# Optimization experiments

Hardware: AMD Instinct MI355X
Metric: run time of the kernel (lower is better)

## Reference

```python
import jax, jax.numpy as jnp
import numpy as np


def setup_inputs() -> dict:
    key = jax.random.key(0)
    k1, k2, k3 = jax.random.split(key, 3)
    N, M, D = 8192, 8192, 64
    return {
        "query": jax.random.normal(k1, (N, D), dtype=jnp.float32),
        "key": jax.random.normal(k2, (M, D), dtype=jnp.float32),
        "value": jax.random.normal(k3, (M, D), dtype=jnp.float32),
        "hyper_c": 1,
        "num_of_method": 2,
    }


def reference(query, key, value, hyper_c, num_of_method):
    # num_of_method == 2 (default): cosine-similarity scores scaled by hyper_c.
    # L2-normalize rows (dim=1), matmul, scale, softmax over keys, weight values.
    q_norm = query / jnp.linalg.norm(query, axis=1, keepdims=True)
    k_norm = key / jnp.linalg.norm(key, axis=1, keepdims=True)
    scores = hyper_c * jnp.einsum("nd,md->nm", q_norm, k_norm)  # [N, M]
    p_attn = jax.nn.softmax(scores, axis=-1)
    res_query = jnp.einsum("nm,md->nd", p_attn, value)  # [N, D]
    return (res_query, p_attn)
```

## Files before the change

### kernel.cpp

```cpp
#include <hip/hip_runtime.h>
#include <hip/hip_bf16.h>
#include <cstdint>
#include <cstddef>

#define NQ 8192
#define NK 8192
#define DD 64
#define KSPLIT 4
#define KRANGE (NK / KSPLIT)
#define KTILE 128

typedef __bf16 bf16x8 __attribute__((ext_vector_type(8)));
typedef float f32x16 __attribute__((ext_vector_type(16)));
typedef unsigned short u16;
typedef uint32_t u32;

static __device__ __forceinline__ u16 f2bf(float f) {
    union { float f; uint32_t u; } v; v.f = f;
    uint32_t r = (v.u + 0x7fffu + ((v.u >> 16) & 1u)) >> 16;
    return (u16)r;
}

static __device__ __forceinline__ u32 cvtpk(float lo, float hi) {
    u32 r;
    asm("v_cvt_pk_bf16_f32 %0, %1, %2" : "=v"(r) : "v"(lo), "v"(hi));
    return r;
}

#define GLOAD16(g, l)                                                          \
    __builtin_amdgcn_global_load_lds(                                          \
        (__attribute__((address_space(1))) void*)(g),                          \
        (__attribute__((address_space(3))) void*)(l), 16, 0, 0)

__global__ void k_norm(const float* __restrict__ q, const float* __restrict__ k,
                       u16* __restrict__ qn, u16* __restrict__ kn) {
    int wid  = (blockIdx.x * blockDim.x + threadIdx.x) >> 6;
    int lane = threadIdx.x & 63;
    int nw   = (gridDim.x * blockDim.x) >> 6;
    for (int row = wid; row < 2 * NQ; row += nw) {
        const float* src = (row < NQ) ? q : k;
        u16* dst = (row < NQ) ? qn : kn;
        int r = row & (NQ - 1);
        float x = src[(size_t)r * DD + lane];
        float ss = x * x;
        #pragma unroll
        for (int m = 1; m < 64; m <<= 1) ss += __shfl_xor(ss, m, 64);
        dst[(size_t)r * DD + lane] = f2bf(x * rsqrtf(ss));
    }
}

__global__ void k_transv(const float* __restrict__ v, u16* __restrict__ vT) {
    __shared__ float ts[64][65];
    int mb = blockIdx.x * 64;
    int t = threadIdx.x;
    #pragma unroll
    for (int i = 0; i < 16; i++) {
        int idx = i * 256 + t;
        int r = idx >> 6, c = idx & 63;
        ts[r][c] = v[(size_t)(mb + r) * DD + c];
    }
    __syncthreads();
    #pragma unroll
    for (int i = 0; i < 16; i++) {
        int idx = i * 256 + t;
        int d = idx >> 6, m = idx & 63;
        vT[(size_t)d * NK + mb + m] = f2bf(ts[m][d]);
    }
}

__global__ __launch_bounds__(256) void
k_flash(const u16* __restrict__ qn, const u16* __restrict__ kn,
        const u16* __restrict__ vT, const int* __restrict__ hcp,
        float* __restrict__ prs, float* __restrict__ ppv) {
    __shared__ __align__(16) u16 qs[32 * 64];
    __shared__ __align__(16) union SmT {
        struct { u16 ks[128 * 64]; u16 vs[64 * 128]; } a;
        struct { float redA[32 * 64]; float redB[32 * 64]; } b;
    } sm;
    __shared__ float rs_ws[4][32];

    const float hc = (float)hcp[0];
    const int t = threadIdx.x;
    const int w = t >> 6;
    const int lane = t & 63;
    const int l31 = lane & 31;
    const int half = lane >> 5;
    const int qb = (blockIdx.x >> 2) * 32;
    const int sp = blockIdx.x & 3;
    const int k0 = sp * KRANGE;
    const int kw = w * 32;

    {
        int row = t >> 3, c = t & 7;
        *reinterpret_cast<uint4*>(&qs[row * 64 + ((c ^ (row & 7)) * 8)]) =
            *reinterpret_cast<const uint4*>(&qn[(size_t)(qb + row) * DD + c * 8]);
    }

    float rs_sum = 0.f;
    f32x16 pv0, pv1;
    #pragma unroll
    for (int i = 0; i < 16; i++) { pv0[i] = 0.f; pv1[i] = 0.f; }

    for (int kb = 0; kb < KRANGE / KTILE; kb++) {
        __syncthreads();
        const u16* ksrc = kn + (size_t)(k0 + kb * KTILE) * DD;
        #pragma unroll
        for (int i = 0; i < 4; i++) {
            int idx16 = (w * 4 + i) * 64 + lane;
            int row = idx16 >> 3, c = idx16 & 7;
            GLOAD16(ksrc + (size_t)row * DD + ((c ^ (row & 7)) * 8),
                    &sm.a.ks[(w * 4 + i) * 512]);
        }
        const u16* vsrc = vT + (size_t)(k0 + kb * KTILE);
        #pragma unroll
        for (int i = 0; i < 4; i++) {
            int idx16 = (w * 4 + i) * 64 + lane;
            int row = idx16 >> 4, c = idx16 & 15;
            GLOAD16(vsrc + (size_t)row * NK + ((c ^ (row & 7)) * 8),
                    &sm.a.vs[(w * 4 + i) * 512]);
        }
        __syncthreads();

        f32x16 acc;
        #pragma unroll
        for (int i = 0; i < 16; i++) acc[i] = 0.f;
        #pragma unroll
        for (int s = 0; s < 4; s++) {
            int ca = 2 * s + half;
            int kr = kw + l31;
            bf16x8 af = *reinterpret_cast<const bf16x8*>(&sm.a.ks[kr * 64 + ((ca ^ (kr & 7)) * 8)]);
            bf16x8 bf = *reinterpret_cast<const bf16x8*>(&qs[l31 * 64 + ((ca ^ (l31 & 7)) * 8)]);
            acc = __builtin_amdgcn_mfma_f32_32x32x16_bf16(af, bf, acc, 0, 0, 0);
        }
        float e[16];
        #pragma unroll
        for (int r = 0; r < 16; r++) {
            e[r] = __expf(acc[r] * hc);
            rs_sum += e[r];
        }
        bf16x8 pa[2];
        #pragma unroll
        for (int s = 0; s < 2; s++) {
            u32 x0 = cvtpk(e[8 * s + 0], e[8 * s + 1]);
            u32 y0 = cvtpk(e[8 * s + 4], e[8 * s + 5]);
            auto r0 = __builtin_amdgcn_permlane32_swap(x0, y0, false, false);
            u32 x1 = cvtpk(e[8 * s + 2], e[8 * s + 3]);
            u32 y1 = cvtpk(e[8 * s + 6], e[8 * s + 7]);
            auto r1 = __builtin_amdgcn_permlane32_swap(x1, y1, false, false);
            union { u32 u[4]; bf16x8 v; } f;
            f.u[0] = r0[0]; f.u[1] = r1[0]; f.u[2] = r0[1]; f.u[3] = r1[1];
            pa[s] = f.v;
        }
        #pragma unroll
        for (int s = 0; s < 2; s++) {
            int cv = (kw >> 3) + 2 * s + half;
            int vr0 = l31, vr1 = 32 + l31;
            bf16x8 b0 = *reinterpret_cast<const bf16x8*>(&sm.a.vs[vr0 * 128 + ((cv ^ (vr0 & 7)) * 8)]);
            bf16x8 b1 = *reinterpret_cast<const bf16x8*>(&sm.a.vs[vr1 * 128 + ((cv ^ (vr1 & 7)) * 8)]);
            pv0 = __builtin_amdgcn_mfma_f32_32x32x16_bf16(pa[s], b0, pv0, 0, 0, 0);
            pv1 = __builtin_amdgcn_mfma_f32_32x32x16_bf16(pa[s], b1, pv1, 0, 0, 0);
        }
    }

    rs_sum += __shfl_xor(rs_sum, 32, 64);
    if (lane < 32) rs_ws[w][lane] = rs_sum;
    __syncthreads();
    if (t < 32)
        prs[(size_t)sp * NQ + qb + t] =
            rs_ws[0][t] + rs_ws[1][t] + rs_ws[2][t] + rs_ws[3][t];

    float* redA = sm.b.redA;
    float* redB = sm.b.redB;
    if (w == 0) {
        #pragma unroll
        for (int r = 0; r < 16; r++) {
            int qq = (r & 3) + 8 * (r >> 2) + 4 * half;
            redA[qq * 64 + l31] = pv0[r];
            redA[qq * 64 + 32 + l31] = pv1[r];
        }
    } else if (w == 1) {
        #pragma unroll
        for (int r = 0; r < 16; r++) {
            int qq = (r & 3) + 8 * (r >> 2) + 4 * half;
            redB[qq * 64 + l31] = pv0[r];
            redB[qq * 64 + 32 + l31] = pv1[r];
        }
    }
    __syncthreads();
    if (w == 2) {
        #pragma unroll
        for (int r = 0; r < 16; r++) {
            int qq = (r & 3) + 8 * (r >> 2) + 4 * half;
            redA[qq * 64 + l31] += pv0[r];
            redA[qq * 64 + 32 + l31] += pv1[r];
        }
    } else if (w == 3) {
        #pragma unroll
        for (int r = 0; r < 16; r++) {
            int qq = (r & 3) + 8 * (r >> 2) + 4 * half;
            redB[qq * 64 + l31] += pv0[r];
            redB[qq * 64 + 32 + l31] += pv1[r];
        }
    }
    __syncthreads();
    float* dst = ppv + (size_t)sp * NQ * DD + (size_t)qb * DD;
    #pragma unroll
    for (int i = 0; i < 8; i++) {
        int idx = i * 256 + t;
        dst[idx] = redA[idx] + redB[idx];
    }
}

__global__ void k_reduce(const float* __restrict__ prs, const float* __restrict__ ppv,
                         float* __restrict__ inv_rs, float* __restrict__ out_res) {
    int id = blockIdx.x * blockDim.x + threadIdx.x;
    int n = id >> 6, d = id & 63;
    float s = prs[n] + prs[NQ + n] + prs[2 * NQ + n] + prs[3 * NQ + n];
    float inv = 1.0f / s;
    if (d == 0) inv_rs[n] = inv;
    const size_t st = (size_t)NQ * DD;
    float v = ppv[id] + ppv[st + id] + ppv[2 * st + id] + ppv[3 * st + id];
    out_res[id] = v * inv;
}

__global__ __launch_bounds__(256) void
k_pwrite(const u16* __restrict__ qn, const u16* __restrict__ kn,
         const float* __restrict__ inv_rs, const int* __restrict__ hcp,
         float* __restrict__ out_p) {
    __shared__ __align__(16) u16 qs2[64 * 64];
    __shared__ __align__(16) u16 ks2[64 * 64];
    __shared__ __align__(16) float pl[64 * 68];
    __shared__ float invl[64];

    const float hc = (float)hcp[0];
    const int bid = blockIdx.x;
    const int qb = (bid >> 7) * 64;
    const int kb = (bid & 127) * 64;
    const int t = threadIdx.x;
    const int w = t >> 6;
    const int lane = t & 63;
    const int l31 = lane & 31;
    const int half = lane >> 5;

    #pragma unroll
    for (int i = 0; i < 2; i++) {
        int idx16 = (w * 2 + i) * 64 + lane;
        int row = idx16 >> 3, c = idx16 & 7;
        GLOAD16(qn + (size_t)(qb + row) * DD + ((c ^ (row & 7)) * 8),
                &qs2[(w * 2 + i) * 512]);
        GLOAD16(kn + (size_t)(kb + row) * DD + ((c ^ (row & 7)) * 8),
                &ks2[(w * 2 + i) * 512]);
    }
    if (t < 64) invl[t] = inv_rs[qb + t];
    __syncthreads();

    const int wq = (w >> 1) * 32, wk = (w & 1) * 32;
    f32x16 acc;
    #pragma unroll
    for (int i = 0; i < 16; i++) acc[i] = 0.f;
    #pragma unroll
    for (int s = 0; s < 4; s++) {
        int ca = 2 * s + half;
        int qr = wq + l31, kr = wk + l31;
        bf16x8 a = *reinterpret_cast<const bf16x8*>(&qs2[qr * 64 + ((ca ^ (qr & 7)) * 8)]);
        bf16x8 b = *reinterpret_cast<const bf16x8*>(&ks2[kr * 64 + ((ca ^ (kr & 7)) * 8)]);
        acc = __builtin_amdgcn_mfma_f32_32x32x16_bf16(a, b, acc, 0, 0, 0);
    }
    #pragma unroll
    for (int r = 0; r < 16; r++) {
        int qq = wq + (r & 3) + 8 * (r >> 2) + 4 * half;
        pl[qq * 68 + wk + l31] = __expf(acc[r] * hc) * invl[qq];
    }
    __syncthreads();
    #pragma unroll
    for (int i = 0; i < 4; i++) {
        int idx = i * 256 + t;
        int row = idx >> 4, c4 = idx & 15;
        float4 vv = *reinterpret_cast<const float4*>(&pl[row * 68 + c4 * 4]);
        *reinterpret_cast<float4*>(&out_p[(size_t)(qb + row) * NK + kb + c4 * 4]) = vv;
    }
}

extern "C" void kernel_launch(void* const* d_in, const int* in_sizes, int n_in,
                              void* d_out, int out_size, void* d_ws, size_t ws_size,
                              hipStream_t stream) {
    const float* q = (const float*)d_in[0];
    const float* k = (const float*)d_in[1];
    const float* v = (const float*)d_in[2];
    const int* hc = (const int*)d_in[3];

    float* out_res = (float*)d_out;
    float* out_p = out_res + (size_t)NQ * DD;

    char* wsb = (char*)d_ws;
    u16* qn = (u16*)wsb;
    u16* kn = qn + (size_t)NQ * DD;
    u16* vT = kn + (size_t)NK * DD;
    float* inv_rs = (float*)(vT + (size_t)NK * DD);

    const size_t base_need = 3 * (size_t)NQ * DD * 2 + (size_t)NQ * 4;
    const size_t extra_need = (size_t)KSPLIT * NQ * 4 + (size_t)KSPLIT * NQ * DD * 4;
    char* extra = (ws_size >= base_need + extra_need)
                      ? wsb + base_need
                      : (char*)out_p + ((size_t)NQ * NK * 4 - extra_need);
    float* prs = (float*)extra;
    float* ppv = prs + (size_t)KSPLIT * NQ;

    k_norm<<<1024, 256, 0, stream>>>(q, k, qn, kn);
    k_transv<<<NK / 64, 256, 0, stream>>>(v, vT);
    k_flash<<<(NQ / 32) * KSPLIT, 256, 0, stream>>>(qn, kn, vT, hc, prs, ppv);
    k_reduce<<<(NQ * DD) / 256, 256, 0, stream>>>(prs, ppv, inv_rs, out_res);
    k_pwrite<<<(NQ / 64) * (NK / 64), 256, 0, stream>>>(qn, kn, inv_rs, hc, out_p);
}
```

Before: 333.8 us.

## Double-buffer K/V tiles in flash kernel and store P directly from registers

The flash kernel now keeps two K/V shared-memory buffers and issues the next tile's loads before computing on the current one, so global loads overlap the MFMA work, with one barrier per iteration instead of two. Doubling the buffers raises LDS use, and launch bounds now ask for 2 blocks per CU. The P-write kernel drops its LDS staging tile and writes exp values straight from MFMA accumulators to global memory with scalar 4-byte stores, and asks for 4 blocks per CU. The direct stores still cover 128-byte row segments per half-wave, but they give up float4 vector stores, which may hurt the bandwidth-bound 256MB P write.

```diff
diff --git a/kernel.cpp b/kernel.cpp
--- a/kernel.cpp
+++ b/kernel.cpp
@@ -9,6 +9,7 @@
 #define KSPLIT 4
 #define KRANGE (NK / KSPLIT)
 #define KTILE 128
+#define NT (KRANGE / KTILE)
 
 typedef __bf16 bf16x8 __attribute__((ext_vector_type(8)));
 typedef float f32x16 __attribute__((ext_vector_type(16)));
@@ -68,14 +69,14 @@
     }
 }
 
-__global__ __launch_bounds__(256) void
+__global__ __launch_bounds__(256, 2) void
 k_flash(const u16* __restrict__ qn, const u16* __restrict__ kn,
         const u16* __restrict__ vT, const int* __restrict__ hcp,
         float* __restrict__ prs, float* __restrict__ ppv) {
     __shared__ __align__(16) u16 qs[32 * 64];
     __shared__ __align__(16) union SmT {
-        struct { u16 ks[128 * 64]; u16 vs[64 * 128]; } a;
-        struct { float redA[32 * 64]; float redB[32 * 64]; } b;
+        struct { u16 ks[128 * 64]; u16 vs[64 * 128]; } t[2];
+        struct { float redA[32 * 64]; float redB[32 * 64]; } ep;
     } sm;
     __shared__ float rs_ws[4][32];
 
@@ -90,6 +91,22 @@
     const int k0 = sp * KRANGE;
     const int kw = w * 32;
 
+#define STAGE_KV(B, KB)                                                        \
+    do {                                                                       \
+        const u16* ksrc_ = kn + (size_t)(k0 + (KB) * KTILE) * DD;              \
+        const u16* vsrc_ = vT + (size_t)(k0 + (KB) * KTILE);                   \
+        _Pragma("unroll")                                                      \
+        for (int i_ = 0; i_ < 4; i_++) {                                       \
+            int idx_ = (w * 4 + i_) * 64 + lane;                               \
+            int kr_ = idx_ >> 3, kc_ = idx_ & 7;                               \
+            GLOAD16(ksrc_ + (size_t)kr_ * DD + ((kc_ ^ (kr_ & 7)) * 8),        \
+                    &sm.t[B].ks[(w * 4 + i_) * 512]);                          \
+            int vr_ = idx_ >> 4, vc_ = idx_ & 15;                              \
+            GLOAD16(vsrc_ + (size_t)vr_ * NK + ((vc_ ^ (vr_ & 7)) * 8),        \
+                    &sm.t[B].vs[(w * 4 + i_) * 512]);                          \
+        }                                                                      \
+    } while (0)
+
     {
         int row = t >> 3, c = t & 7;
         *reinterpret_cast<uint4*>(&qs[row * 64 + ((c ^ (row & 7)) * 8)]) =
@@ -101,25 +118,15 @@
     #pragma unroll
     for (int i = 0; i < 16; i++) { pv0[i] = 0.f; pv1[i] = 0.f; }
 
-    for (int kb = 0; kb < KRANGE / KTILE; kb++) {
-        __syncthreads();
-        const u16* ksrc = kn + (size_t)(k0 + kb * KTILE) * DD;
-        #pragma unroll
-        for (int i = 0; i < 4; i++) {
-            int idx16 = (w * 4 + i) * 64 + lane;
-            int row = idx16 >> 3, c = idx16 & 7;
-            GLOAD16(ksrc + (size_t)row * DD + ((c ^ (row & 7)) * 8),
-                    &sm.a.ks[(w * 4 + i) * 512]);
-        }
-        const u16* vsrc = vT + (size_t)(k0 + kb * KTILE);
-        #pragma unroll
-        for (int i = 0; i < 4; i++) {
-            int idx16 = (w * 4 + i) * 64 + lane;
-            int row = idx16 >> 4, c = idx16 & 15;
-            GLOAD16(vsrc + (size_t)row * NK + ((c ^ (row & 7)) * 8),
-                    &sm.a.vs[(w * 4 + i) * 512]);
-        }
-        __syncthreads();
+    STAGE_KV(0, 0);
+    __syncthreads();
+
+    int cur = 0;
+    for (int kb = 0; kb < NT; kb++) {
+        if (kb + 1 < NT) STAGE_KV(cur ^ 1, kb + 1);
+
+        const u16* ks_ = sm.t[cur].ks;
+        const u16* vs_ = sm.t[cur].vs;
 
         f32x16 acc;
         #pragma unroll
@@ -128,7 +135,7 @@
         for (int s = 0; s < 4; s++) {
             int ca = 2 * s + half;
             int kr = kw + l31;
-            bf16x8 af = *reinterpret_cast<const bf16x8*>(&sm.a.ks[kr * 64 + ((ca ^ (kr & 7)) * 8)]);
+            bf16x8 af = *reinterpret_cast<const bf16x8*>(&ks_[kr * 64 + ((ca ^ (kr & 7)) * 8)]);
             bf16x8 bf = *reinterpret_cast<const bf16x8*>(&qs[l31 * 64 + ((ca ^ (l31 & 7)) * 8)]);
             acc = __builtin_amdgcn_mfma_f32_32x32x16_bf16(af, bf, acc, 0, 0, 0);
         }
@@ -155,11 +162,14 @@
         for (int s = 0; s < 2; s++) {
             int cv = (kw >> 3) + 2 * s + half;
             int vr0 = l31, vr1 = 32 + l31;
-            bf16x8 b0 = *reinterpret_cast<const bf16x8*>(&sm.a.vs[vr0 * 128 + ((cv ^ (vr0 & 7)) * 8)]);
-            bf16x8 b1 = *reinterpret_cast<const bf16x8*>(&sm.a.vs[vr1 * 128 + ((cv ^ (vr1 & 7)) * 8)]);
+            bf16x8 b0 = *reinterpret_cast<const bf16x8*>(&vs_[vr0 * 128 + ((cv ^ (vr0 & 7)) * 8)]);
+            bf16x8 b1 = *reinterpret_cast<const bf16x8*>(&vs_[vr1 * 128 + ((cv ^ (vr1 & 7)) * 8)]);
             pv0 = __builtin_amdgcn_mfma_f32_32x32x16_bf16(pa[s], b0, pv0, 0, 0, 0);
             pv1 = __builtin_amdgcn_mfma_f32_32x32x16_bf16(pa[s], b1, pv1, 0, 0, 0);
         }
+
+        __syncthreads();
+        cur ^= 1;
     }
 
     rs_sum += __shfl_xor(rs_sum, 32, 64);
@@ -169,8 +179,8 @@
         prs[(size_t)sp * NQ + qb + t] =
             rs_ws[0][t] + rs_ws[1][t] + rs_ws[2][t] + rs_ws[3][t];
 
-    float* redA = sm.b.redA;
-    float* redB = sm.b.redB;
+    float* redA = sm.ep.redA;
+    float* redB = sm.ep.redB;
     if (w == 0) {
         #pragma unroll
         for (int r = 0; r < 16; r++) {
@@ -209,6 +219,7 @@
         int idx = i * 256 + t;
         dst[idx] = redA[idx] + redB[idx];
     }
+#undef STAGE_KV
 }
 
 __global__ void k_reduce(const float* __restrict__ prs, const float* __restrict__ ppv,
@@ -223,13 +234,12 @@
     out_res[id] = v * inv;
 }
 
-__global__ __launch_bounds__(256) void
+__global__ __launch_bounds__(256, 4) void
 k_pwrite(const u16* __restrict__ qn, const u16* __restrict__ kn,
          const float* __restrict__ inv_rs, const int* __restrict__ hcp,
          float* __restrict__ out_p) {
     __shared__ __align__(16) u16 qs2[64 * 64];
     __shared__ __align__(16) u16 ks2[64 * 64];
-    __shared__ __align__(16) float pl[64 * 68];
     __shared__ float invl[64];
 
     const float hc = (float)hcp[0];
@@ -269,15 +279,7 @@
     #pragma unroll
     for (int r = 0; r < 16; r++) {
         int qq = wq + (r & 3) + 8 * (r >> 2) + 4 * half;
-        pl[qq * 68 + wk + l31] = __expf(acc[r] * hc) * invl[qq];
-    }
-    __syncthreads();
-    #pragma unroll
-    for (int i = 0; i < 4; i++) {
-        int idx = i * 256 + t;
-        int row = idx >> 4, c4 = idx & 15;
-        float4 vv = *reinterpret_cast<const float4*>(&pl[row * 68 + c4 * 4]);
-        *reinterpret_cast<float4*>(&out_p[(size_t)(qb + row) * NK + kb + c4 * 4]) = vv;
+        out_p[(size_t)(qb + qq) * NK + kb + wk + l31] = __expf(acc[r] * hc) * invl[qq];
     }
 }
 
```

Measured after the change: 334.8 us. Within noise of the previous version (+0.3%).
